# Performance work log

Hardware: AMD Instinct MI355X
Metric: run time of the kernel (lower is better)

The kernel has to match this reference:

```python
import jax, jax.numpy as jnp
import numpy as np

DILATION = 3
HC_MULT = 4
HIDDEN_DIM = 32
ENGRAM_DIM = 32
KERNEL_SIZE = 4
EPS = 1.1920929e-07  # torch RMSNorm default eps=None -> finfo(fp32).eps


def rmsnorm(x, w):
    # x: [..., C], w broadcastable to x
    ms = jnp.mean(x * x, axis=-1, keepdims=True)
    return x * jax.lax.rsqrt(ms + EPS) * w


def setup_inputs() -> dict:
    key = jax.random.key(0)
    ks = jax.random.split(key, 12)
    B, T = 16, 8192
    s = 0.05
    return {
        "embeddings": jax.random.normal(ks[0], (B, T, ENGRAM_DIM), jnp.float32),
        "hidden_states": jax.random.normal(ks[1], (B, T, HC_MULT, HIDDEN_DIM), jnp.float32),
        "Wv": jax.random.normal(ks[2], (HIDDEN_DIM, ENGRAM_DIM), jnp.float32) * s,
        "bv": jax.random.normal(ks[3], (HIDDEN_DIM,), jnp.float32) * s,
        "Wk": jax.random.normal(ks[4], (HC_MULT, HIDDEN_DIM, ENGRAM_DIM), jnp.float32) * s,
        "bk": jax.random.normal(ks[5], (HC_MULT, HIDDEN_DIM), jnp.float32) * s,
        "n1_w": jnp.ones((HC_MULT, HIDDEN_DIM), jnp.float32),
        "n2_w": jnp.ones((HC_MULT, HIDDEN_DIM), jnp.float32),
        "cn_w": jnp.ones((HC_MULT, HIDDEN_DIM), jnp.float32),
        "conv_w": jax.random.normal(ks[6], (HC_MULT * HIDDEN_DIM, 1, KERNEL_SIZE), jnp.float32) * s,
    }


def reference(embeddings, hidden_states, Wv, bv, Wk, bk, n1_w, n2_w, cn_w, conv_w):
    B, T, G, C = hidden_states.shape
    # per-branch key projection: [B,T,G,C]
    key = jnp.einsum("btd,gcd->btgc", embeddings, Wk) + bk
    normed_key = rmsnorm(key, n1_w)                    # [B,T,G,C]
    normed_query = rmsnorm(hidden_states, n2_w)        # [B,T,G,C]
    gate = jnp.sum(normed_key * normed_query, axis=-1) / np.sqrt(C)  # [B,T,G]
    gate = jnp.sqrt(jnp.maximum(jnp.abs(gate), 1e-6)) * jnp.sign(gate)
    gate = jax.nn.sigmoid(gate)[..., None]             # [B,T,G,1]
    value = (embeddings @ Wv.T + bv)[:, :, None, :]    # [B,T,1,C]
    gated = gate * value                               # [B,T,G,C]
    # per-branch RMSNorm then concat channels
    x_norm = rmsnorm(gated, cn_w).reshape(B, T, G * C)
    x_bct = jnp.transpose(x_norm, (0, 2, 1))           # [B, G*C, T]
    pad = (KERNEL_SIZE - 1) * DILATION                 # causal left pad = 9
    y_bct = jax.lax.conv_general_dilated(
        x_bct, conv_w,
        window_strides=(1,), padding=[(pad, 0)],
        rhs_dilation=(DILATION,),
        dimension_numbers=("NCH", "OIH", "NCH"),
        feature_group_count=G * C,
    )
    y_bct = jax.nn.silu(y_bct)
    conv_out = jnp.transpose(y_bct, (0, 2, 1)).reshape(B, T, G, C)
    return gated + conv_out
```

## Files before the change

kernel.cpp:

```cpp
#include <hip/hip_runtime.h>
#include <hip/hip_fp16.h>

#define TT    64
#define HALO  9
#define NTOK  73
#define XSTR  132
#define VSTR  36
#define EPS   1.1920929e-07f

typedef __attribute__((ext_vector_type(8))) _Float16 f16x8;
typedef __attribute__((ext_vector_type(4))) float f32x4;

template<int CTRL>
__device__ __forceinline__ float dpp_add(float x) {
    int y = __builtin_amdgcn_update_dpp(0, __float_as_int(x), CTRL, 0xF, 0xF, true);
    return x + __int_as_float(y);
}
__device__ __forceinline__ float redsum16(float x) {
    x = dpp_add<0x128>(x);
    x = dpp_add<0x124>(x);
    x = dpp_add<0x122>(x);
    x = dpp_add<0x121>(x);
    return x;
}

__device__ __forceinline__ float fast_rcp(float x) {
    return __builtin_amdgcn_rcpf(x);
}

extern "C" __global__ __launch_bounds__(256)
void engram_norm(const float* __restrict__ emb,
                 const float* __restrict__ hid,
                 const float* __restrict__ Wv,
                 const float* __restrict__ bv,
                 const float* __restrict__ Wk,
                 const float* __restrict__ bk,
                 const float* __restrict__ n1w,
                 const float* __restrict__ n2w,
                 const float* __restrict__ cnw,
                 __half* __restrict__ xn_out,
                 float* __restrict__ val_out,
                 float* __restrict__ gate_out)
{
    const int tid  = threadIdx.x;
    const int b    = blockIdx.x >> 7;
    const int tile = blockIdx.x & 127;
    const int t0   = tile * 64;

    const int wv  = tid >> 6;
    const int ln  = tid & 63;
    const int l15 = ln & 15;
    const int q   = ln >> 4;
    const int tw  = t0 + wv * 16;

    float2 q2[4][4];
    #pragma unroll
    for (int r = 0; r < 4; ++r) {
        const int t = tw + q * 4 + r;
        const float2* qp = (const float2*)&hid[(size_t)((b << 13) + t) * 128];
        #pragma unroll
        for (int g = 0; g < 4; ++g) q2[r][g] = qp[g * 16 + l15];
    }

    float4 f0, f1;
    {
        const float4* p = (const float4*)&emb[(size_t)((b << 13) + tw + l15) * 32 + q * 8];
        f0 = p[0];
        f1 = p[1];
    }

    const float2 bv2 = ((const float2*)bv)[l15];
    float2 bk2[4], wn1[4], wn2[4], wcn[4];
    #pragma unroll
    for (int g = 0; g < 4; ++g) {
        bk2[g] = ((const float2*)(bk  + g * 32))[l15];
        wn1[g] = ((const float2*)(n1w + g * 32))[l15];
        wn2[g] = ((const float2*)(n2w + g * 32))[l15];
        wcn[g] = ((const float2*)(cnw + g * 32))[l15];
    }

    f16x8 a;
    a[0] = (_Float16)f0.x; a[1] = (_Float16)f0.y;
    a[2] = (_Float16)f0.z; a[3] = (_Float16)f0.w;
    a[4] = (_Float16)f1.x; a[5] = (_Float16)f1.y;
    a[6] = (_Float16)f1.z; a[7] = (_Float16)f1.w;

    f32x4 D[10];
    #pragma unroll
    for (int nt = 0; nt < 10; ++nt) {
        const int e = nt & 1, p = nt >> 1;
        const int ch = 2 * l15 + e;
        const float* wrow = (p == 0) ? &Wv[ch * 32] : &Wk[((p - 1) * 32 + ch) * 32];
        float4 w0 = ((const float4*)wrow)[q * 2];
        float4 w1 = ((const float4*)wrow)[q * 2 + 1];
        f16x8 bf;
        bf[0] = (_Float16)w0.x; bf[1] = (_Float16)w0.y;
        bf[2] = (_Float16)w0.z; bf[3] = (_Float16)w0.w;
        bf[4] = (_Float16)w1.x; bf[5] = (_Float16)w1.y;
        bf[6] = (_Float16)w1.z; bf[7] = (_Float16)w1.w;
        const float bias = (p == 0) ? (e ? bv2.y : bv2.x)
                                    : (e ? bk2[p - 1].y : bk2[p - 1].x);
        f32x4 c = {bias, bias, bias, bias};
        D[nt] = __builtin_amdgcn_mfma_f32_16x16x32_f16(a, bf, c, 0, 0, 0);
    }

    #pragma unroll
    for (int r = 0; r < 4; ++r) {
        const int ti = tw + q * 4 + r;
        const float V0 = D[0][r], V1 = D[1][r];
        float msv = redsum16(V0 * V0 + V1 * V1);
        float gs[4];
        float xnv[4][2];
        #pragma unroll
        for (int g = 0; g < 4; ++g) {
            const float K0 = D[2 + 2 * g][r], K1v = D[3 + 2 * g][r];
            const float q0 = q2[r][g].x, q1 = q2[r][g].y;
            float msk = redsum16(K0 * K0 + K1v * K1v);
            float msq = redsum16(q0 * q0 + q1 * q1);
            float dr  = redsum16(K0 * wn1[g].x * q0 * wn2[g].x
                               + K1v * wn1[g].y * q1 * wn2[g].y);
            float rk = rsqrtf(msk * (1.f / 32.f) + EPS);
            float rq = rsqrtf(msq * (1.f / 32.f) + EPS);
            float dot = dr * rk * rq * 0.17677669529663689f;
            float sa = sqrtf(fmaxf(fabsf(dot), 1e-6f));
            float gate = fast_rcp(1.f + __expf(-copysignf(sa, dot)));
            gs[g] = gate;
            float sc = gate * rsqrtf(gate * gate * msv * (1.f / 32.f) + EPS);
            xnv[g][0] = sc * V0 * wcn[g].x;
            xnv[g][1] = sc * V1 * wcn[g].y;
        }
        __half* xrow = xn_out + (size_t)((b << 13) + ti) * 128;
        #pragma unroll
        for (int g = 0; g < 4; ++g) {
            *(__half2*)&xrow[g * 32 + 2 * l15] = __floats2half2_rn(xnv[g][0], xnv[g][1]);
        }
        *(float2*)&val_out[(size_t)((b << 13) + ti) * 32 + 2 * l15] = make_float2(V0, V1);
        if (l15 < 4) {
            float gsel = (l15 == 0) ? gs[0] : (l15 == 1) ? gs[1]
                       : (l15 == 2) ? gs[2] : gs[3];
            gate_out[(size_t)((b << 13) + ti) * 4 + l15] = gsel;
        }
    }
}

extern "C" __global__ __launch_bounds__(256)
void engram_conv(const __half* __restrict__ xn,
                 const float* __restrict__ val,
                 const float* __restrict__ gate,
                 const float* __restrict__ cw,
                 float* __restrict__ out)
{
    const int gid = blockIdx.x * 256 + threadIdx.x;
    const int c4i = gid & 31;
    const int c4  = c4i << 2;
    const int t   = (gid >> 5) & 8191;
    const int b   = gid >> 18;
    const int g   = c4 >> 5;

    const float4* cw4p = (const float4*)cw;
    const float4 w0 = cw4p[c4 + 0];
    const float4 w1 = cw4p[c4 + 1];
    const float4 w2 = cw4p[c4 + 2];
    const float4 w3 = cw4p[c4 + 3];

    const size_t row = (size_t)((b << 13) + t);
    float y0 = 0.f, y1 = 0.f, y2 = 0.f, y3 = 0.f;
    #pragma unroll
    for (int k = 0; k < 4; ++k) {
        const int tp  = t - HALO + 3 * k;
        const float m = (tp >= 0) ? 1.f : 0.f;
        const int tpc = tp < 0 ? 0 : tp;
        const __half2* xp = (const __half2*)&xn[(size_t)((b << 13) + tpc) * 128 + c4];
        float2 a01 = __half22float2(xp[0]);
        float2 a23 = __half22float2(xp[1]);
        const float wk0 = (k == 0) ? w0.x : (k == 1) ? w0.y : (k == 2) ? w0.z : w0.w;
        const float wk1 = (k == 0) ? w1.x : (k == 1) ? w1.y : (k == 2) ? w1.z : w1.w;
        const float wk2 = (k == 0) ? w2.x : (k == 1) ? w2.y : (k == 2) ? w2.z : w2.w;
        const float wk3 = (k == 0) ? w3.x : (k == 1) ? w3.y : (k == 2) ? w3.z : w3.w;
        y0 = fmaf(m * a01.x, wk0, y0);
        y1 = fmaf(m * a01.y, wk1, y1);
        y2 = fmaf(m * a23.x, wk2, y2);
        y3 = fmaf(m * a23.y, wk3, y3);
    }
    const float gg = gate[row * 4 + g];
    const f32x4 v  = *(const f32x4*)&val[row * 32 + (c4 & 31)];
    float4 o;
    o.x = gg * v[0] + y0 * fast_rcp(1.f + __expf(-y0));
    o.y = gg * v[1] + y1 * fast_rcp(1.f + __expf(-y1));
    o.z = gg * v[2] + y2 * fast_rcp(1.f + __expf(-y2));
    o.w = gg * v[3] + y3 * fast_rcp(1.f + __expf(-y3));
    *(float4*)&out[row * 128 + c4] = o;
}

extern "C" __global__ __launch_bounds__(320, 3)
void engram_fused(const float* __restrict__ emb,
                  const float* __restrict__ hid,
                  const float* __restrict__ Wv,
                  const float* __restrict__ bv,
                  const float* __restrict__ Wk,
                  const float* __restrict__ bk,
                  const float* __restrict__ n1w,
                  const float* __restrict__ n2w,
                  const float* __restrict__ cnw,
                  const float* __restrict__ cw,
                  float* __restrict__ out)
{
    __shared__ __align__(16) __half s_xn[NTOK * XSTR];
    __shared__ __align__(16) float  s_val[TT * VSTR];
    __shared__ float  s_gate[TT * 4];

    const int tid  = threadIdx.x;
    const int b    = blockIdx.x >> 7;
    const int tile = blockIdx.x & 127;
    const int t0   = tile * TT;

    const int wv  = tid >> 6;
    const int ln  = tid & 63;
    const int l15 = ln & 15;
    const int q   = ln >> 4;
    const int ibase = wv * 16 + q * 4;

    float2 q2[4][4];
    float  okm[4];
    #pragma unroll
    for (int r = 0; r < 4; ++r) {
        int t = t0 - HALO + ibase + r;
        okm[r] = (t >= 0 && t < 8192) ? 1.f : 0.f;
        int tc = t < 0 ? 0 : (t > 8191 ? 8191 : t);
        const float2* qp = (const float2*)&hid[(size_t)((b << 13) + tc) * 128];
        #pragma unroll
        for (int g = 0; g < 4; ++g) q2[r][g] = qp[g * 16 + l15];
    }

    float4 f0, f1;
    float amask;
    {
        const int tA = t0 - HALO + wv * 16 + l15;
        amask = (tA >= 0 && tA < 8192) ? 1.f : 0.f;
        const int tAc = tA < 0 ? 0 : (tA > 8191 ? 8191 : tA);
        const float4* p = (const float4*)&emb[(size_t)((b << 13) + tAc) * 32 + q * 8];
        f0 = p[0];
        f1 = p[1];
    }

    const float2 bv2 = ((const float2*)bv)[l15];
    float2 bk2[4], wn1[4], wn2[4], wcn[4];
    #pragma unroll
    for (int g = 0; g < 4; ++g) {
        bk2[g] = ((const float2*)(bk  + g * 32))[l15];
        wn1[g] = ((const float2*)(n1w + g * 32))[l15];
        wn2[g] = ((const float2*)(n2w + g * 32))[l15];
        wcn[g] = ((const float2*)(cnw + g * 32))[l15];
    }

    f16x8 a;
    a[0] = (_Float16)(amask * f0.x); a[1] = (_Float16)(amask * f0.y);
    a[2] = (_Float16)(amask * f0.z); a[3] = (_Float16)(amask * f0.w);
    a[4] = (_Float16)(amask * f1.x); a[5] = (_Float16)(amask * f1.y);
    a[6] = (_Float16)(amask * f1.z); a[7] = (_Float16)(amask * f1.w);

    f32x4 D[10];
    #pragma unroll
    for (int nt = 0; nt < 10; ++nt) {
        const int e = nt & 1, p = nt >> 1;
        const int ch = 2 * l15 + e;
        const float* wrow = (p == 0) ? &Wv[ch * 32] : &Wk[((p - 1) * 32 + ch) * 32];
        float4 w0 = ((const float4*)wrow)[q * 2];
        float4 w1 = ((const float4*)wrow)[q * 2 + 1];
        f16x8 bf;
        bf[0] = (_Float16)w0.x; bf[1] = (_Float16)w0.y;
        bf[2] = (_Float16)w0.z; bf[3] = (_Float16)w0.w;
        bf[4] = (_Float16)w1.x; bf[5] = (_Float16)w1.y;
        bf[6] = (_Float16)w1.z; bf[7] = (_Float16)w1.w;
        const float bias = (p == 0) ? (e ? bv2.y : bv2.x)
                                    : (e ? bk2[p - 1].y : bk2[p - 1].x);
        f32x4 c = {bias, bias, bias, bias};
        D[nt] = __builtin_amdgcn_mfma_f32_16x16x32_f16(a, bf, c, 0, 0, 0);
    }

    #pragma unroll
    for (int r = 0; r < 4; ++r) {
        const int i = ibase + r;
        const float V0 = D[0][r], V1 = D[1][r];
        float msv = redsum16(V0 * V0 + V1 * V1);
        float gs[4];
        float xnv[4][2];
        #pragma unroll
        for (int g = 0; g < 4; ++g) {
            const float K0 = D[2 + 2 * g][r], K1v = D[3 + 2 * g][r];
            const float q0 = q2[r][g].x * okm[r], q1 = q2[r][g].y * okm[r];
            float msk = redsum16(K0 * K0 + K1v * K1v);
            float msq = redsum16(q0 * q0 + q1 * q1);
            float dr  = redsum16(K0 * wn1[g].x * q0 * wn2[g].x
                               + K1v * wn1[g].y * q1 * wn2[g].y);
            float rk = rsqrtf(msk * (1.f / 32.f) + EPS);
            float rq = rsqrtf(msq * (1.f / 32.f) + EPS);
            float dot = dr * rk * rq * 0.17677669529663689f;
            float sa = sqrtf(fmaxf(fabsf(dot), 1e-6f));
            float gate = fast_rcp(1.f + __expf(-copysignf(sa, dot)));
            gs[g] = gate;
            float sc = gate * rsqrtf(gate * gate * msv * (1.f / 32.f) + EPS);
            xnv[g][0] = sc * V0 * wcn[g].x;
            xnv[g][1] = sc * V1 * wcn[g].y;
        }
        if (i < NTOK) {
            #pragma unroll
            for (int g = 0; g < 4; ++g) {
                __half2 h2 = __floats2half2_rn(okm[r] * xnv[g][0], okm[r] * xnv[g][1]);
                *(__half2*)&s_xn[i * XSTR + g * 32 + 2 * l15] = h2;
            }
            if (i >= HALO) {
                const int j = i - HALO;
                *(float2*)&s_val[j * VSTR + 2 * l15] = make_float2(V0, V1);
                if (l15 < 4) {
                    float gsel = (l15 == 0) ? gs[0] : (l15 == 1) ? gs[1]
                               : (l15 == 2) ? gs[2] : gs[3];
                    s_gate[j * 4 + l15] = gsel;
                }
            }
        }
    }
    __syncthreads();

    const float4* cw4p = (const float4*)cw;
    for (int idx = tid; idx < TT * 32; idx += 320) {
        const int j  = idx >> 5;
        const int c4 = (idx & 31) << 2;
        float4 w0 = cw4p[c4 + 0];
        float4 w1 = cw4p[c4 + 1];
        float4 w2 = cw4p[c4 + 2];
        float4 w3 = cw4p[c4 + 3];
        float y0 = 0.f, y1 = 0.f, y2 = 0.f, y3 = 0.f;
        #pragma unroll
        for (int k = 0; k < 4; ++k) {
            const __half2* xp = (const __half2*)&s_xn[(j + 3 * k) * XSTR + c4];
            float2 a01 = __half22float2(xp[0]);
            float2 a23 = __half22float2(xp[1]);
            const float wk0 = (k == 0) ? w0.x : (k == 1) ? w0.y : (k == 2) ? w0.z : w0.w;
            const float wk1 = (k == 0) ? w1.x : (k == 1) ? w1.y : (k == 2) ? w1.z : w1.w;
            const float wk2 = (k == 0) ? w2.x : (k == 1) ? w2.y : (k == 2) ? w2.z : w2.w;
            const float wk3 = (k == 0) ? w3.x : (k == 1) ? w3.y : (k == 2) ? w3.z : w3.w;
            y0 = fmaf(a01.x, wk0, y0);
            y1 = fmaf(a01.y, wk1, y1);
            y2 = fmaf(a23.x, wk2, y2);
            y3 = fmaf(a23.y, wk3, y3);
        }
        const float g  = s_gate[j * 4 + (c4 >> 5)];
        const f32x4 v  = *(const f32x4*)&s_val[j * VSTR + (c4 & 31)];
        float4 o;
        o.x = g * v[0] + y0 * fast_rcp(1.f + __expf(-y0));
        o.y = g * v[1] + y1 * fast_rcp(1.f + __expf(-y1));
        o.z = g * v[2] + y2 * fast_rcp(1.f + __expf(-y2));
        o.w = g * v[3] + y3 * fast_rcp(1.f + __expf(-y3));
        *(float4*)&out[(size_t)((b << 13) + t0 + j) * 128 + c4] = o;
    }
}

extern "C" void kernel_launch(void* const* d_in, const int* in_sizes, int n_in,
                              void* d_out, int out_size, void* d_ws, size_t ws_size,
                              hipStream_t stream) {
    const float* emb = (const float*)d_in[0];
    const float* hid = (const float*)d_in[1];
    const float* Wv  = (const float*)d_in[2];
    const float* bvp = (const float*)d_in[3];
    const float* Wk  = (const float*)d_in[4];
    const float* bkp = (const float*)d_in[5];
    const float* n1  = (const float*)d_in[6];
    const float* n2  = (const float*)d_in[7];
    const float* cn  = (const float*)d_in[8];
    const float* cwp = (const float*)d_in[9];
    float* out = (float*)d_out;

    const size_t xn_bytes   = (size_t)16 * 8192 * 128 * sizeof(__half);
    const size_t val_bytes  = (size_t)16 * 8192 * 32 * sizeof(float);
    const size_t gate_bytes = (size_t)16 * 8192 * 4 * sizeof(float);
    const size_t need = xn_bytes + val_bytes + gate_bytes;

    if (d_ws != nullptr && ws_size >= need) {
        __half* xn  = (__half*)d_ws;
        float* val  = (float*)((char*)d_ws + xn_bytes);
        float* gate = (float*)((char*)d_ws + xn_bytes + val_bytes);
        engram_norm<<<dim3(16 * 128), dim3(256), 0, stream>>>(
            emb, hid, Wv, bvp, Wk, bkp, n1, n2, cn, xn, val, gate);
        engram_conv<<<dim3(16 * 8192 * 32 / 256), dim3(256), 0, stream>>>(
            xn, val, gate, cwp, out);
    } else {
        engram_fused<<<dim3(16 * 128), dim3(320), 0, stream>>>(
            emb, hid, Wv, bvp, Wk, bkp, n1, n2, cn, cwp, out);
    }
}
```

Before: 181.2 us.

## Make norm and conv kernels persistent with double-buffered tile prefetch

The norm kernel now runs a fixed grid of 512 blocks, each handling four tiles, and uses two register buffers so the next tile's hidden/embedding loads are in flight while the current tile computes. The conv kernel now runs 2048 blocks that each loop over 8 slabs, and it loads the four halves as one float2. The aim is to amortise per-block weight loads and launch overhead and to overlap memory latency with compute. In exchange register pressure rises from holding two tiles, and fewer waves are resident to hide latency.

```diff
diff --git a/kernel.cpp b/kernel.cpp
--- a/kernel.cpp
+++ b/kernel.cpp
@@ -8,6 +8,11 @@
 #define VSTR  36
 #define EPS   1.1920929e-07f
 
+#define NTILES 2048
+#define GRID1  512
+#define GRID2  2048
+#define K2_SLAB (GRID2 * 256)
+
 typedef __attribute__((ext_vector_type(8))) _Float16 f16x8;
 typedef __attribute__((ext_vector_type(4))) float f32x4;
 
@@ -28,7 +33,109 @@
     return __builtin_amdgcn_rcpf(x);
 }
 
-extern "C" __global__ __launch_bounds__(256)
+struct TileIn {
+    float2 q2[4][4];
+    float4 f0, f1;
+};
+
+struct Wgt {
+    float2 bv2;
+    float2 bk2[4], wn1[4], wn2[4], wcn[4];
+};
+
+__device__ __forceinline__ void tile_load(TileIn& T,
+                                          const float* __restrict__ emb,
+                                          const float* __restrict__ hid,
+                                          int tileIdx, int wv, int l15, int q) {
+    const int b  = tileIdx >> 7;
+    const int tw = (tileIdx & 127) * 64 + wv * 16;
+    #pragma unroll
+    for (int r = 0; r < 4; ++r) {
+        const int t = tw + q * 4 + r;
+        const float2* qp = (const float2*)&hid[(size_t)((b << 13) + t) * 128];
+        #pragma unroll
+        for (int g = 0; g < 4; ++g) T.q2[r][g] = qp[g * 16 + l15];
+    }
+    const float4* p = (const float4*)&emb[(size_t)((b << 13) + tw + l15) * 32 + q * 8];
+    T.f0 = p[0];
+    T.f1 = p[1];
+}
+
+__device__ __forceinline__ void tile_compute(const TileIn& T, const Wgt& W,
+                                             const float* __restrict__ Wv,
+                                             const float* __restrict__ Wk,
+                                             __half* __restrict__ xn_out,
+                                             float* __restrict__ val_out,
+                                             float* __restrict__ gate_out,
+                                             int tileIdx, int wv, int l15, int q) {
+    const int b  = tileIdx >> 7;
+    const int tw = (tileIdx & 127) * 64 + wv * 16;
+
+    f16x8 a;
+    a[0] = (_Float16)T.f0.x; a[1] = (_Float16)T.f0.y;
+    a[2] = (_Float16)T.f0.z; a[3] = (_Float16)T.f0.w;
+    a[4] = (_Float16)T.f1.x; a[5] = (_Float16)T.f1.y;
+    a[6] = (_Float16)T.f1.z; a[7] = (_Float16)T.f1.w;
+
+    f32x4 D[10];
+    #pragma unroll
+    for (int nt = 0; nt < 10; ++nt) {
+        const int e = nt & 1, p = nt >> 1;
+        const int ch = 2 * l15 + e;
+        const float* wrow = (p == 0) ? &Wv[ch * 32] : &Wk[((p - 1) * 32 + ch) * 32];
+        float4 w0 = ((const float4*)wrow)[q * 2];
+        float4 w1 = ((const float4*)wrow)[q * 2 + 1];
+        f16x8 bf;
+        bf[0] = (_Float16)w0.x; bf[1] = (_Float16)w0.y;
+        bf[2] = (_Float16)w0.z; bf[3] = (_Float16)w0.w;
+        bf[4] = (_Float16)w1.x; bf[5] = (_Float16)w1.y;
+        bf[6] = (_Float16)w1.z; bf[7] = (_Float16)w1.w;
+        const float bias = (p == 0) ? (e ? W.bv2.y : W.bv2.x)
+                                    : (e ? W.bk2[p - 1].y : W.bk2[p - 1].x);
+        f32x4 c = {bias, bias, bias, bias};
+        D[nt] = __builtin_amdgcn_mfma_f32_16x16x32_f16(a, bf, c, 0, 0, 0);
+    }
+
+    #pragma unroll
+    for (int r = 0; r < 4; ++r) {
+        const int ti = tw + q * 4 + r;
+        const float V0 = D[0][r], V1 = D[1][r];
+        float msv = redsum16(V0 * V0 + V1 * V1);
+        float gs[4];
+        float xnv[4][2];
+        #pragma unroll
+        for (int g = 0; g < 4; ++g) {
+            const float K0 = D[2 + 2 * g][r], K1v = D[3 + 2 * g][r];
+            const float q0 = T.q2[r][g].x, q1 = T.q2[r][g].y;
+            float msk = redsum16(K0 * K0 + K1v * K1v);
+            float msq = redsum16(q0 * q0 + q1 * q1);
+            float dr  = redsum16(K0 * W.wn1[g].x * q0 * W.wn2[g].x
+                               + K1v * W.wn1[g].y * q1 * W.wn2[g].y);
+            float rk = rsqrtf(msk * (1.f / 32.f) + EPS);
+            float rq = rsqrtf(msq * (1.f / 32.f) + EPS);
+            float dot = dr * rk * rq * 0.17677669529663689f;
+            float sa = sqrtf(fmaxf(fabsf(dot), 1e-6f));
+            float gate = fast_rcp(1.f + __expf(-copysignf(sa, dot)));
+            gs[g] = gate;
+            float sc = gate * rsqrtf(gate * gate * msv * (1.f / 32.f) + EPS);
+            xnv[g][0] = sc * V0 * W.wcn[g].x;
+            xnv[g][1] = sc * V1 * W.wcn[g].y;
+        }
+        __half* xrow = xn_out + (size_t)((b << 13) + ti) * 128;
+        #pragma unroll
+        for (int g = 0; g < 4; ++g) {
+            *(__half2*)&xrow[g * 32 + 2 * l15] = __floats2half2_rn(xnv[g][0], xnv[g][1]);
+        }
+        *(float2*)&val_out[(size_t)((b << 13) + ti) * 32 + 2 * l15] = make_float2(V0, V1);
+        if (l15 < 4) {
+            float gsel = (l15 == 0) ? gs[0] : (l15 == 1) ? gs[1]
+                       : (l15 == 2) ? gs[2] : gs[3];
+            gate_out[(size_t)((b << 13) + ti) * 4 + l15] = gsel;
+        }
+    }
+}
+
+extern "C" __global__ __launch_bounds__(256, 2)
 void engram_norm(const float* __restrict__ emb,
                  const float* __restrict__ hid,
                  const float* __restrict__ Wv,
@@ -42,105 +149,32 @@
                  float* __restrict__ val_out,
                  float* __restrict__ gate_out)
 {
-    const int tid  = threadIdx.x;
-    const int b    = blockIdx.x >> 7;
-    const int tile = blockIdx.x & 127;
-    const int t0   = tile * 64;
-
+    const int tid = threadIdx.x;
     const int wv  = tid >> 6;
     const int ln  = tid & 63;
     const int l15 = ln & 15;
     const int q   = ln >> 4;
-    const int tw  = t0 + wv * 16;
-
-    float2 q2[4][4];
-    #pragma unroll
-    for (int r = 0; r < 4; ++r) {
-        const int t = tw + q * 4 + r;
-        const float2* qp = (const float2*)&hid[(size_t)((b << 13) + t) * 128];
-        #pragma unroll
-        for (int g = 0; g < 4; ++g) q2[r][g] = qp[g * 16 + l15];
-    }
-
-    float4 f0, f1;
-    {
-        const float4* p = (const float4*)&emb[(size_t)((b << 13) + tw + l15) * 32 + q * 8];
-        f0 = p[0];
-        f1 = p[1];
-    }
-
-    const float2 bv2 = ((const float2*)bv)[l15];
-    float2 bk2[4], wn1[4], wn2[4], wcn[4];
+
+    Wgt W;
+    W.bv2 = ((const float2*)bv)[l15];
     #pragma unroll
     for (int g = 0; g < 4; ++g) {
-        bk2[g] = ((const float2*)(bk  + g * 32))[l15];
-        wn1[g] = ((const float2*)(n1w + g * 32))[l15];
-        wn2[g] = ((const float2*)(n2w + g * 32))[l15];
-        wcn[g] = ((const float2*)(cnw + g * 32))[l15];
-    }
-
-    f16x8 a;
-    a[0] = (_Float16)f0.x; a[1] = (_Float16)f0.y;
-    a[2] = (_Float16)f0.z; a[3] = (_Float16)f0.w;
-    a[4] = (_Float16)f1.x; a[5] = (_Float16)f1.y;
-    a[6] = (_Float16)f1.z; a[7] = (_Float16)f1.w;
-
-    f32x4 D[10];
-    #pragma unroll
-    for (int nt = 0; nt < 10; ++nt) {
-        const int e = nt & 1, p = nt >> 1;
-        const int ch = 2 * l15 + e;
-        const float* wrow = (p == 0) ? &Wv[ch * 32] : &Wk[((p - 1) * 32 + ch) * 32];
-        float4 w0 = ((const float4*)wrow)[q * 2];
-        float4 w1 = ((const float4*)wrow)[q * 2 + 1];
-        f16x8 bf;
-        bf[0] = (_Float16)w0.x; bf[1] = (_Float16)w0.y;
-        bf[2] = (_Float16)w0.z; bf[3] = (_Float16)w0.w;
-        bf[4] = (_Float16)w1.x; bf[5] = (_Float16)w1.y;
-        bf[6] = (_Float16)w1.z; bf[7] = (_Float16)w1.w;
-        const float bias = (p == 0) ? (e ? bv2.y : bv2.x)
-                                    : (e ? bk2[p - 1].y : bk2[p - 1].x);
-        f32x4 c = {bias, bias, bias, bias};
-        D[nt] = __builtin_amdgcn_mfma_f32_16x16x32_f16(a, bf, c, 0, 0, 0);
-    }
-
-    #pragma unroll
-    for (int r = 0; r < 4; ++r) {
-        const int ti = tw + q * 4 + r;
-        const float V0 = D[0][r], V1 = D[1][r];
-        float msv = redsum16(V0 * V0 + V1 * V1);
-        float gs[4];
-        float xnv[4][2];
-        #pragma unroll
-        for (int g = 0; g < 4; ++g) {
-            const float K0 = D[2 + 2 * g][r], K1v = D[3 + 2 * g][r];
-            const float q0 = q2[r][g].x, q1 = q2[r][g].y;
-            float msk = redsum16(K0 * K0 + K1v * K1v);
-            float msq = redsum16(q0 * q0 + q1 * q1);
-            float dr  = redsum16(K0 * wn1[g].x * q0 * wn2[g].x
-                               + K1v * wn1[g].y * q1 * wn2[g].y);
-            float rk = rsqrtf(msk * (1.f / 32.f) + EPS);
-            float rq = rsqrtf(msq * (1.f / 32.f) + EPS);
-            float dot = dr * rk * rq * 0.17677669529663689f;
-            float sa = sqrtf(fmaxf(fabsf(dot), 1e-6f));
-            float gate = fast_rcp(1.f + __expf(-copysignf(sa, dot)));
-            gs[g] = gate;
-            float sc = gate * rsqrtf(gate * gate * msv * (1.f / 32.f) + EPS);
-            xnv[g][0] = sc * V0 * wcn[g].x;
-            xnv[g][1] = sc * V1 * wcn[g].y;
-        }
-        __half* xrow = xn_out + (size_t)((b << 13) + ti) * 128;
-        #pragma unroll
-        for (int g = 0; g < 4; ++g) {
-            *(__half2*)&xrow[g * 32 + 2 * l15] = __floats2half2_rn(xnv[g][0], xnv[g][1]);
-        }
-        *(float2*)&val_out[(size_t)((b << 13) + ti) * 32 + 2 * l15] = make_float2(V0, V1);
-        if (l15 < 4) {
-            float gsel = (l15 == 0) ? gs[0] : (l15 == 1) ? gs[1]
-                       : (l15 == 2) ? gs[2] : gs[3];
-            gate_out[(size_t)((b << 13) + ti) * 4 + l15] = gsel;
-        }
-    }
+        W.bk2[g] = ((const float2*)(bk  + g * 32))[l15];
+        W.wn1[g] = ((const float2*)(n1w + g * 32))[l15];
+        W.wn2[g] = ((const float2*)(n2w + g * 32))[l15];
+        W.wcn[g] = ((const float2*)(cnw + g * 32))[l15];
+    }
+
+    const int i0 = blockIdx.x;
+    TileIn A, B;
+    tile_load(A, emb, hid, i0,             wv, l15, q);
+    tile_load(B, emb, hid, i0 + GRID1,     wv, l15, q);
+    tile_compute(A, W, Wv, Wk, xn_out, val_out, gate_out, i0,             wv, l15, q);
+    tile_load(A, emb, hid, i0 + 2 * GRID1, wv, l15, q);
+    tile_compute(B, W, Wv, Wk, xn_out, val_out, gate_out, i0 + GRID1,     wv, l15, q);
+    tile_load(B, emb, hid, i0 + 3 * GRID1, wv, l15, q);
+    tile_compute(A, W, Wv, Wk, xn_out, val_out, gate_out, i0 + 2 * GRID1, wv, l15, q);
+    tile_compute(B, W, Wv, Wk, xn_out, val_out, gate_out, i0 + 3 * GRID1, wv, l15, q);
 }
 
 extern "C" __global__ __launch_bounds__(256)
@@ -150,11 +184,8 @@
                  const float* __restrict__ cw,
                  float* __restrict__ out)
 {
-    const int gid = blockIdx.x * 256 + threadIdx.x;
-    const int c4i = gid & 31;
-    const int c4  = c4i << 2;
-    const int t   = (gid >> 5) & 8191;
-    const int b   = gid >> 18;
+    const int tid = threadIdx.x;
+    const int c4  = (tid & 31) << 2;
     const int g   = c4 >> 5;
 
     const float4* cw4p = (const float4*)cw;
@@ -163,33 +194,40 @@
     const float4 w2 = cw4p[c4 + 2];
     const float4 w3 = cw4p[c4 + 3];
 
-    const size_t row = (size_t)((b << 13) + t);
-    float y0 = 0.f, y1 = 0.f, y2 = 0.f, y3 = 0.f;
-    #pragma unroll
-    for (int k = 0; k < 4; ++k) {
-        const int tp  = t - HALO + 3 * k;
-        const float m = (tp >= 0) ? 1.f : 0.f;
-        const int tpc = tp < 0 ? 0 : tp;
-        const __half2* xp = (const __half2*)&xn[(size_t)((b << 13) + tpc) * 128 + c4];
-        float2 a01 = __half22float2(xp[0]);
-        float2 a23 = __half22float2(xp[1]);
-        const float wk0 = (k == 0) ? w0.x : (k == 1) ? w0.y : (k == 2) ? w0.z : w0.w;
-        const float wk1 = (k == 0) ? w1.x : (k == 1) ? w1.y : (k == 2) ? w1.z : w1.w;
-        const float wk2 = (k == 0) ? w2.x : (k == 1) ? w2.y : (k == 2) ? w2.z : w2.w;
-        const float wk3 = (k == 0) ? w3.x : (k == 1) ? w3.y : (k == 2) ? w3.z : w3.w;
-        y0 = fmaf(m * a01.x, wk0, y0);
-        y1 = fmaf(m * a01.y, wk1, y1);
-        y2 = fmaf(m * a23.x, wk2, y2);
-        y3 = fmaf(m * a23.y, wk3, y3);
-    }
-    const float gg = gate[row * 4 + g];
-    const f32x4 v  = *(const f32x4*)&val[row * 32 + (c4 & 31)];
-    float4 o;
-    o.x = gg * v[0] + y0 * fast_rcp(1.f + __expf(-y0));
-    o.y = gg * v[1] + y1 * fast_rcp(1.f + __expf(-y1));
-    o.z = gg * v[2] + y2 * fast_rcp(1.f + __expf(-y2));
-    o.w = gg * v[3] + y3 * fast_rcp(1.f + __expf(-y3));
-    *(float4*)&out[row * 128 + c4] = o;
+    int gid = blockIdx.x * 256 + tid;
+    #pragma unroll
+    for (int it = 0; it < 8; ++it, gid += K2_SLAB) {
+        const int t = (gid >> 5) & 8191;
+        const int b = gid >> 18;
+        const size_t row = (size_t)((b << 13) + t);
+
+        float y0 = 0.f, y1 = 0.f, y2 = 0.f, y3 = 0.f;
+        #pragma unroll
+        for (int k = 0; k < 4; ++k) {
+            const int tp  = t - HALO + 3 * k;
+            const float m = (tp >= 0) ? 1.f : 0.f;
+            const int tpc = tp < 0 ? 0 : tp;
+            const float2 rv = *(const float2*)&xn[(size_t)((b << 13) + tpc) * 128 + c4];
+            float2 a01 = __half22float2(*(const __half2*)&rv.x);
+            float2 a23 = __half22float2(*(const __half2*)&rv.y);
+            const float wk0 = (k == 0) ? w0.x : (k == 1) ? w0.y : (k == 2) ? w0.z : w0.w;
+            const float wk1 = (k == 0) ? w1.x : (k == 1) ? w1.y : (k == 2) ? w1.z : w1.w;
+            const float wk2 = (k == 0) ? w2.x : (k == 1) ? w2.y : (k == 2) ? w2.z : w2.w;
+            const float wk3 = (k == 0) ? w3.x : (k == 1) ? w3.y : (k == 2) ? w3.z : w3.w;
+            y0 = fmaf(m * a01.x, wk0, y0);
+            y1 = fmaf(m * a01.y, wk1, y1);
+            y2 = fmaf(m * a23.x, wk2, y2);
+            y3 = fmaf(m * a23.y, wk3, y3);
+        }
+        const float gg = gate[row * 4 + g];
+        const f32x4 v  = *(const f32x4*)&val[row * 32 + (c4 & 31)];
+        float4 o;
+        o.x = gg * v[0] + y0 * fast_rcp(1.f + __expf(-y0));
+        o.y = gg * v[1] + y1 * fast_rcp(1.f + __expf(-y1));
+        o.z = gg * v[2] + y2 * fast_rcp(1.f + __expf(-y2));
+        o.w = gg * v[3] + y3 * fast_rcp(1.f + __expf(-y3));
+        *(float4*)&out[row * 128 + c4] = o;
+    }
 }
 
 extern "C" __global__ __launch_bounds__(320, 3)
@@ -380,9 +418,9 @@
         __half* xn  = (__half*)d_ws;
         float* val  = (float*)((char*)d_ws + xn_bytes);
         float* gate = (float*)((char*)d_ws + xn_bytes + val_bytes);
-        engram_norm<<<dim3(16 * 128), dim3(256), 0, stream>>>(
+        engram_norm<<<dim3(GRID1), dim3(256), 0, stream>>>(
             emb, hid, Wv, bvp, Wk, bkp, n1, n2, cn, xn, val, gate);
-        engram_conv<<<dim3(16 * 8192 * 32 / 256), dim3(256), 0, stream>>>(
+        engram_conv<<<dim3(GRID2), dim3(256), 0, stream>>>(
             xn, val, gate, cwp, out);
     } else {
         engram_fused<<<dim3(16 * 128), dim3(320), 0, stream>>>(
```

Result: slower. 193.4 us (+6.7%).

## Prepack fp16 weight fragments and reuse conv taps across four timesteps per thread

Applied to the files above, without the earlier changes.

Adds a tiny prep kernel that converts Wv/Wk into fp16 MFMA B-fragments once, so the norm kernel loads one 16-byte vector per tile instead of converting fp32 weights in every block. The conv kernel now gives each thread four outputs spaced by the dilation and loads 7 shared taps instead of 16 separate ones, cutting redundant reads of xn. It also merges two rsqrt calls into one. The cost is an extra kernel launch, integer div/mod index math and more registers in the conv kernel.

```diff
diff --git a/kernel.cpp b/kernel.cpp
--- a/kernel.cpp
+++ b/kernel.cpp
@@ -8,6 +8,10 @@
 #define VSTR  36
 #define EPS   1.1920929e-07f
 
+#define GRID1  2048
+#define NM     683
+#define GRID2  4098
+
 typedef __attribute__((ext_vector_type(8))) _Float16 f16x8;
 typedef __attribute__((ext_vector_type(4))) float f32x4;
 
@@ -28,16 +32,36 @@
     return __builtin_amdgcn_rcpf(x);
 }
 
+extern "C" __global__ __launch_bounds__(640)
+void engram_prep(const float* __restrict__ Wv,
+                 const float* __restrict__ Wk,
+                 __half* __restrict__ wfrag)
+{
+    const int idx = threadIdx.x;
+    const int nt  = idx >> 6;
+    const int l15 = (idx >> 2) & 15;
+    const int q   = idx & 3;
+    const int e = nt & 1, p = nt >> 1;
+    const int ch = 2 * l15 + e;
+    const float* wrow = (p == 0) ? &Wv[ch * 32] : &Wk[((p - 1) * 32 + ch) * 32];
+    float4 w0 = ((const float4*)wrow)[q * 2];
+    float4 w1 = ((const float4*)wrow)[q * 2 + 1];
+    __half2* dst = (__half2*)(wfrag + (size_t)idx * 8);
+    dst[0] = __floats2half2_rn(w0.x, w0.y);
+    dst[1] = __floats2half2_rn(w0.z, w0.w);
+    dst[2] = __floats2half2_rn(w1.x, w1.y);
+    dst[3] = __floats2half2_rn(w1.z, w1.w);
+}
+
 extern "C" __global__ __launch_bounds__(256)
 void engram_norm(const float* __restrict__ emb,
                  const float* __restrict__ hid,
-                 const float* __restrict__ Wv,
                  const float* __restrict__ bv,
-                 const float* __restrict__ Wk,
                  const float* __restrict__ bk,
                  const float* __restrict__ n1w,
                  const float* __restrict__ n2w,
                  const float* __restrict__ cnw,
+                 const __half* __restrict__ wfrag,
                  __half* __restrict__ xn_out,
                  float* __restrict__ val_out,
                  float* __restrict__ gate_out)
@@ -85,19 +109,12 @@
     a[4] = (_Float16)f1.x; a[5] = (_Float16)f1.y;
     a[6] = (_Float16)f1.z; a[7] = (_Float16)f1.w;
 
+    const f16x8* wf = (const f16x8*)wfrag;
     f32x4 D[10];
     #pragma unroll
     for (int nt = 0; nt < 10; ++nt) {
         const int e = nt & 1, p = nt >> 1;
-        const int ch = 2 * l15 + e;
-        const float* wrow = (p == 0) ? &Wv[ch * 32] : &Wk[((p - 1) * 32 + ch) * 32];
-        float4 w0 = ((const float4*)wrow)[q * 2];
-        float4 w1 = ((const float4*)wrow)[q * 2 + 1];
-        f16x8 bf;
-        bf[0] = (_Float16)w0.x; bf[1] = (_Float16)w0.y;
-        bf[2] = (_Float16)w0.z; bf[3] = (_Float16)w0.w;
-        bf[4] = (_Float16)w1.x; bf[5] = (_Float16)w1.y;
-        bf[6] = (_Float16)w1.z; bf[7] = (_Float16)w1.w;
+        f16x8 bf = wf[nt * 64 + l15 * 4 + q];
         const float bias = (p == 0) ? (e ? bv2.y : bv2.x)
                                     : (e ? bk2[p - 1].y : bk2[p - 1].x);
         f32x4 c = {bias, bias, bias, bias};
@@ -119,9 +136,8 @@
             float msq = redsum16(q0 * q0 + q1 * q1);
             float dr  = redsum16(K0 * wn1[g].x * q0 * wn2[g].x
                                + K1v * wn1[g].y * q1 * wn2[g].y);
-            float rk = rsqrtf(msk * (1.f / 32.f) + EPS);
-            float rq = rsqrtf(msq * (1.f / 32.f) + EPS);
-            float dot = dr * rk * rq * 0.17677669529663689f;
+            float rkq = rsqrtf((msk * (1.f / 32.f) + EPS) * (msq * (1.f / 32.f) + EPS));
+            float dot = dr * rkq * 0.17677669529663689f;
             float sa = sqrtf(fmaxf(fabsf(dot), 1e-6f));
             float gate = fast_rcp(1.f + __expf(-copysignf(sa, dot)));
             gs[g] = gate;
@@ -153,9 +169,13 @@
     const int gid = blockIdx.x * 256 + threadIdx.x;
     const int c4i = gid & 31;
     const int c4  = c4i << 2;
-    const int t   = (gid >> 5) & 8191;
-    const int b   = gid >> 18;
     const int g   = c4 >> 5;
+    int rest = gid >> 5;
+    const int m  = rest % NM;
+    rest /= NM;
+    const int r  = rest % 3;
+    const int b  = rest / 3;
+    const int t0 = 12 * m + r;
 
     const float4* cw4p = (const float4*)cw;
     const float4 w0 = cw4p[c4 + 0];
@@ -163,33 +183,46 @@
     const float4 w2 = cw4p[c4 + 2];
     const float4 w3 = cw4p[c4 + 3];
 
-    const size_t row = (size_t)((b << 13) + t);
-    float y0 = 0.f, y1 = 0.f, y2 = 0.f, y3 = 0.f;
-    #pragma unroll
-    for (int k = 0; k < 4; ++k) {
-        const int tp  = t - HALO + 3 * k;
-        const float m = (tp >= 0) ? 1.f : 0.f;
-        const int tpc = tp < 0 ? 0 : tp;
-        const __half2* xp = (const __half2*)&xn[(size_t)((b << 13) + tpc) * 128 + c4];
+    float2 tap01[7], tap23[7];
+    #pragma unroll
+    for (int j = 0; j < 7; ++j) {
+        const int tr = t0 - 9 + 3 * j;
+        const float mj = (tr >= 0) ? 1.f : 0.f;
+        const int trc = tr < 0 ? 0 : (tr > 8191 ? 8191 : tr);
+        const __half2* xp = (const __half2*)&xn[(size_t)((b << 13) + trc) * 128 + c4];
         float2 a01 = __half22float2(xp[0]);
         float2 a23 = __half22float2(xp[1]);
-        const float wk0 = (k == 0) ? w0.x : (k == 1) ? w0.y : (k == 2) ? w0.z : w0.w;
-        const float wk1 = (k == 0) ? w1.x : (k == 1) ? w1.y : (k == 2) ? w1.z : w1.w;
-        const float wk2 = (k == 0) ? w2.x : (k == 1) ? w2.y : (k == 2) ? w2.z : w2.w;
-        const float wk3 = (k == 0) ? w3.x : (k == 1) ? w3.y : (k == 2) ? w3.z : w3.w;
-        y0 = fmaf(m * a01.x, wk0, y0);
-        y1 = fmaf(m * a01.y, wk1, y1);
-        y2 = fmaf(m * a23.x, wk2, y2);
-        y3 = fmaf(m * a23.y, wk3, y3);
-    }
-    const float gg = gate[row * 4 + g];
-    const f32x4 v  = *(const f32x4*)&val[row * 32 + (c4 & 31)];
-    float4 o;
-    o.x = gg * v[0] + y0 * fast_rcp(1.f + __expf(-y0));
-    o.y = gg * v[1] + y1 * fast_rcp(1.f + __expf(-y1));
-    o.z = gg * v[2] + y2 * fast_rcp(1.f + __expf(-y2));
-    o.w = gg * v[3] + y3 * fast_rcp(1.f + __expf(-y3));
-    *(float4*)&out[row * 128 + c4] = o;
+        tap01[j] = make_float2(mj * a01.x, mj * a01.y);
+        tap23[j] = make_float2(mj * a23.x, mj * a23.y);
+    }
+
+    #pragma unroll
+    for (int i = 0; i < 4; ++i) {
+        const int t = t0 + 3 * i;
+        if (t < 8192) {
+            float y0 = 0.f, y1 = 0.f, y2 = 0.f, y3 = 0.f;
+            #pragma unroll
+            for (int k = 0; k < 4; ++k) {
+                const float wk0 = (k == 0) ? w0.x : (k == 1) ? w0.y : (k == 2) ? w0.z : w0.w;
+                const float wk1 = (k == 0) ? w1.x : (k == 1) ? w1.y : (k == 2) ? w1.z : w1.w;
+                const float wk2 = (k == 0) ? w2.x : (k == 1) ? w2.y : (k == 2) ? w2.z : w2.w;
+                const float wk3 = (k == 0) ? w3.x : (k == 1) ? w3.y : (k == 2) ? w3.z : w3.w;
+                y0 = fmaf(tap01[i + k].x, wk0, y0);
+                y1 = fmaf(tap01[i + k].y, wk1, y1);
+                y2 = fmaf(tap23[i + k].x, wk2, y2);
+                y3 = fmaf(tap23[i + k].y, wk3, y3);
+            }
+            const size_t row = (size_t)((b << 13) + t);
+            const float gg = gate[row * 4 + g];
+            const f32x4 v  = *(const f32x4*)&val[row * 32 + (c4 & 31)];
+            float4 o;
+            o.x = gg * v[0] + y0 * fast_rcp(1.f + __expf(-y0));
+            o.y = gg * v[1] + y1 * fast_rcp(1.f + __expf(-y1));
+            o.z = gg * v[2] + y2 * fast_rcp(1.f + __expf(-y2));
+            o.w = gg * v[3] + y3 * fast_rcp(1.f + __expf(-y3));
+            *(float4*)&out[row * 128 + c4] = o;
+        }
+    }
 }
 
 extern "C" __global__ __launch_bounds__(320, 3)
@@ -374,15 +407,18 @@
     const size_t xn_bytes   = (size_t)16 * 8192 * 128 * sizeof(__half);
     const size_t val_bytes  = (size_t)16 * 8192 * 32 * sizeof(float);
     const size_t gate_bytes = (size_t)16 * 8192 * 4 * sizeof(float);
-    const size_t need = xn_bytes + val_bytes + gate_bytes;
+    const size_t wf_bytes   = (size_t)640 * 8 * sizeof(__half);
+    const size_t need = xn_bytes + val_bytes + gate_bytes + wf_bytes;
 
     if (d_ws != nullptr && ws_size >= need) {
         __half* xn  = (__half*)d_ws;
         float* val  = (float*)((char*)d_ws + xn_bytes);
         float* gate = (float*)((char*)d_ws + xn_bytes + val_bytes);
-        engram_norm<<<dim3(16 * 128), dim3(256), 0, stream>>>(
-            emb, hid, Wv, bvp, Wk, bkp, n1, n2, cn, xn, val, gate);
-        engram_conv<<<dim3(16 * 8192 * 32 / 256), dim3(256), 0, stream>>>(
+        __half* wf  = (__half*)((char*)d_ws + xn_bytes + val_bytes + gate_bytes);
+        engram_prep<<<dim3(1), dim3(640), 0, stream>>>(Wv, Wk, wf);
+        engram_norm<<<dim3(GRID1), dim3(256), 0, stream>>>(
+            emb, hid, bvp, bkp, n1, n2, cn, wf, xn, val, gate);
+        engram_conv<<<dim3(GRID2), dim3(256), 0, stream>>>(
             xn, val, gate, cwp, out);
     } else {
         engram_fused<<<dim3(16 * 128), dim3(320), 0, stream>>>(
```

Result: faster. 167.0 us (-7.8%).
